# Optimization experiments

Hardware: AMD Instinct MI355X
Metric: run time of the kernel (lower is better)

Reference implementation:

```python
import jax, jax.numpy as jnp
import numpy as np

# Problem sizes
N, D, B = 4096, 2048, 64  # nodes, feature dim, sequential samples
# LARFDSSOM hyperparameters (from __init__ defaults)
A_T = 0.3          # activation threshold
DSBETA = 1e-4      # moving-average rate
E_B = 0.5          # winner learning rate
E_N = 0.01 * E_B   # neighbor learning rate (e_n is multiplied by e_b in __init__)
EPS_DS = 0.01      # relevance smoothing


def setup_inputs() -> dict:
    key = jax.random.key(0)
    k0, k1, k2, k3, k4 = jax.random.split(key, 5)
    return {
        "x": jax.random.uniform(k0, (B, D), jnp.float32),
        "weights": jax.random.uniform(k1, (N, D), jnp.float32),
        "moving_avg": jax.random.uniform(k2, (N, D), jnp.float32),
        "relevances": jax.random.uniform(k3, (N, D), jnp.float32),
        "wins": jnp.zeros((N,), jnp.float32),
        "neighbors": jax.random.randint(k4, (N, N), 0, 2) > 0,
    }


def _som_steps(x, weights, moving_avg, relevances, wins, neighbors):
    """Sequential LARFDSSOM update_map over B samples (codebook at max size,
    so the add_node branch is structurally impossible and the per-sample step
    is either 'update winner + neighbors' or a no-op)."""
    node_ids = jnp.arange(weights.shape[0])

    def step(state, w):
        W, M, R, wn = state
        diff = w[None, :] - W                          # [N, D]
        # weighted_distance + activation
        dists = jnp.sum(R * diff * diff, axis=1)       # [N]
        rel_sum = jnp.sum(R, axis=1)                   # [N]
        act = rel_sum / (rel_sum + dists + 1e-7)
        winner = jnp.argmax(act)
        do_upd = act[winner] >= A_T                    # else no-op (codebook full)
        is_winner = node_ids == winner
        is_nb = neighbors[winner] & (~is_winner)
        # per-node learning rate: e_b for winner, e_n for neighbors, 0 otherwise
        lr = jnp.where(is_winner, E_B, jnp.where(is_nb, E_N, 0.0))[:, None]  # [N, 1]
        # update_node (vectorized over all nodes, masked below)
        dist_abs = jnp.abs(diff)
        M_new = lr * DSBETA * dist_abs + (1.0 - lr * DSBETA) * M
        mx = jnp.max(M_new, axis=1, keepdims=True)
        mn = jnp.min(M_new, axis=1, keepdims=True)
        av = jnp.mean(M_new, axis=1, keepdims=True)
        denom = EPS_DS * (mx - mn)
        # denom == 0 -> original produces NaN then sets relevance to 1.0
        arg = jnp.clip((M_new - av) / jnp.where(denom == 0.0, 1.0, denom), -80.0, 80.0)
        R_new = jnp.where(denom == 0.0, 1.0, 1.0 / (1.0 + jnp.exp(arg)))
        W_new = W + lr * diff
        m = (do_upd & (lr[:, 0] > 0.0))[:, None]       # rows actually touched
        W = jnp.where(m, W_new, W)
        M = jnp.where(m, M_new, M)
        R = jnp.where(m, R_new, R)
        wn = wn + jnp.where(is_winner & do_upd, 1.0, 0.0)
        return (W, M, R, wn), None

    (W, M, R, wn), _ = jax.lax.scan(step, (weights, moving_avg, relevances, wins), x)
    return W


def reference(x, weights, moving_avg, relevances, wins, neighbors):
    return _som_steps(x, weights, moving_avg, relevances, wins, neighbors)
```

## Files before the change

### kernel.cpp

```cpp
#include <hip/hip_runtime.h>
#include <cstddef>

#define NN 4096
#define DD 2048
#define BB 64
#define RPB 8
#define NBLK (NN / RPB)

constexpr float kAT     = 0.3f;
constexpr float kDSBETA = 1e-4f;
constexpr float kEB     = 0.5f;
constexpr float kEN     = 0.005f;
constexpr float kEPS    = 0.01f;

__device__ __forceinline__ float wave_sum_f(float v) {
#pragma unroll
    for (int o = 32; o; o >>= 1) v += __shfl_xor(v, o, 64);
    return v;
}
__device__ __forceinline__ double wave_sum_d(double v) {
#pragma unroll
    for (int o = 32; o; o >>= 1) v += __shfl_xor(v, o, 64);
    return v;
}
__device__ __forceinline__ float wave_max_f(float v) {
#pragma unroll
    for (int o = 32; o; o >>= 1) v = fmaxf(v, __shfl_xor(v, o, 64));
    return v;
}
__device__ __forceinline__ float wave_min_f(float v) {
#pragma unroll
    for (int o = 32; o; o >>= 1) v = fminf(v, __shfl_xor(v, o, 64));
    return v;
}
__device__ __forceinline__ unsigned long long wave_max_u64(unsigned long long v) {
#pragma unroll
    for (int o = 32; o; o >>= 1) {
        const unsigned long long u = __shfl_xor(v, o, 64);
        v = (u > v) ? u : v;
    }
    return v;
}

__global__ void detect_nb(const unsigned char* __restrict__ nb, unsigned* __restrict__ flag) {
    unsigned v = 0;
    const int i0 = threadIdx.x * 256;
    for (int i = 0; i < 256; i++) {
        const int idx = i0 + i;
        if ((idx & 3) != 0) v |= nb[idx];
    }
    if (v != 0) atomicOr(flag, 1u);
}

__global__ __launch_bounds__(256, 2) void som_persist(
    const float* __restrict__ x,
    const float* __restrict__ W0,
    const float* __restrict__ M0,
    const float* __restrict__ R0,
    const unsigned char* __restrict__ nbb,
    const unsigned* __restrict__ flag,
    float* __restrict__ Wout,
    unsigned long long* __restrict__ part,
    unsigned* __restrict__ cnt)
{
    const int tid  = threadIdx.x;
    const int wid  = tid >> 6;
    const int lane = tid & 63;
    const int n0   = (int)blockIdx.x * RPB;
    const int col  = tid * 8;

    __shared__ double sdd[2][RPB][4];
    __shared__ float  sf[3][4];
    __shared__ unsigned long long skk[RPB];
    __shared__ unsigned long long sKey;

    const bool nb_byte = (*flag != 0);
    const int* nbi = (const int*)nbb;

    float w[RPB][8], r[RPB][8], m[RPB][8], xcur[8];

#pragma unroll
    for (int row = 0; row < RPB; ++row) {
        const size_t base = (size_t)(n0 + row) * DD + col;
        *(float4*)(&w[row][0]) = *(const float4*)(W0 + base);
        *(float4*)(&w[row][4]) = *(const float4*)(W0 + base + 4);
        *(float4*)(&r[row][0]) = *(const float4*)(R0 + base);
        *(float4*)(&r[row][4]) = *(const float4*)(R0 + base + 4);
        *(float4*)(&m[row][0]) = *(const float4*)(M0 + base);
        *(float4*)(&m[row][4]) = *(const float4*)(M0 + base + 4);
    }
    *(float4*)(xcur)     = *(const float4*)(x + col);
    *(float4*)(xcur + 4) = *(const float4*)(x + col + 4);

    auto act_phase = [&](int slot) {
#pragma unroll
        for (int row = 0; row < RPB; ++row) {
            double pd = 0.0, ps = 0.0;
#pragma unroll
            for (int j = 0; j < 8; ++j) {
                const double d  = (double)xcur[j] - (double)w[row][j];
                const double rj = (double)r[row][j];
                pd += rj * d * d;
                ps += rj;
            }
            pd = wave_sum_d(pd); ps = wave_sum_d(ps);
            if (lane == 0) { sdd[0][row][wid] = pd; sdd[1][row][wid] = ps; }
        }
        __syncthreads();
        if (tid < RPB) {
            const int row = tid;
            const double td = sdd[0][row][0] + sdd[0][row][1] + sdd[0][row][2] + sdd[0][row][3];
            const double tr = sdd[1][row][0] + sdd[1][row][1] + sdd[1][row][2] + sdd[1][row][3];
            const double act = tr / (tr + td + 1e-7);
            const unsigned long long ab = (unsigned long long)__double_as_longlong(act);
            skk[row] = (ab & ~0xFFFULL) | (unsigned long long)(4095 - (n0 + row));
        }
        __syncthreads();
        if (tid == 0) {
            unsigned long long k = skk[0];
#pragma unroll
            for (int i = 1; i < RPB; ++i) k = (skk[i] > k) ? skk[i] : k;
            atomicMax(&part[((size_t)slot * 64 + (blockIdx.x & 63)) * 8], k);
            __hip_atomic_fetch_add(&cnt[((size_t)slot * 8 + (blockIdx.x & 7)) * 16], 1u,
                                   __ATOMIC_RELEASE, __HIP_MEMORY_SCOPE_AGENT);
        }
        __syncthreads();
    };

    act_phase(0);

    for (int t = 0; t < BB; ++t) {
        if (wid == 0) {
            int it = 0;
            while (true) {
                unsigned c = 0;
                if (lane < 8)
                    c = __hip_atomic_load(&cnt[((size_t)t * 8 + lane) * 16],
                                          __ATOMIC_ACQUIRE, __HIP_MEMORY_SCOPE_AGENT);
                c += __shfl_xor(c, 1, 64);
                c += __shfl_xor(c, 2, 64);
                c += __shfl_xor(c, 4, 64);
                c = __shfl(c, 0, 64);
                if (c >= (unsigned)NBLK) break;
                if (++it > 2000000) break;
                __builtin_amdgcn_s_sleep(2);
            }
            unsigned long long k = __hip_atomic_load(
                &part[((size_t)t * 64 + lane) * 8],
                __ATOMIC_RELAXED, __HIP_MEMORY_SCOPE_AGENT);
            k = wave_max_u64(k);
            if (lane == 0) sKey = k;
        }
        __syncthreads();
        const unsigned long long k = sKey;
        __syncthreads();
        const double act_w = __longlong_as_double((long long)(k & ~0xFFFULL));
        const int winner   = 4095 - (int)(k & 0xFFFULL);

        if (act_w >= (double)kAT) {
#pragma unroll
            for (int row = 0; row < RPB; ++row) {
                const int n = n0 + row;
                float lr = 0.0f;
                if (n == winner) {
                    lr = kEB;
                } else {
                    const size_t off = (size_t)winner * NN + n;
                    const bool isnb = nb_byte ? (nbb[off] != 0) : (nbi[off] != 0);
                    if (isnb) lr = kEN;
                }
                if (lr != 0.0f) {
                    const float c1 = lr * kDSBETA;
                    const float c2 = 1.0f - c1;
                    float psum = 0.0f, pmx = -INFINITY, pmn = INFINITY;
#pragma unroll
                    for (int j = 0; j < 8; ++j) {
                        const float d  = xcur[j] - w[row][j];
                        const float mv = c1 * fabsf(d) + c2 * m[row][j];
                        w[row][j] += lr * d;
                        m[row][j] = mv;
                        psum += mv;
                        pmx = fmaxf(pmx, mv);
                        pmn = fminf(pmn, mv);
                    }
                    psum = wave_sum_f(psum); pmx = wave_max_f(pmx); pmn = wave_min_f(pmn);
                    if (lane == 0) { sf[0][wid] = psum; sf[1][wid] = pmx; sf[2][wid] = pmn; }
                    __syncthreads();
                    const float ts  = sf[0][0] + sf[0][1] + sf[0][2] + sf[0][3];
                    const float tmx = fmaxf(fmaxf(sf[1][0], sf[1][1]), fmaxf(sf[1][2], sf[1][3]));
                    const float tmn = fminf(fminf(sf[2][0], sf[2][1]), fminf(sf[2][2], sf[2][3]));
                    __syncthreads();
                    const float av    = ts * (1.0f / (float)DD);
                    const float denom = kEPS * (tmx - tmn);
                    if (denom == 0.0f) {
#pragma unroll
                        for (int j = 0; j < 8; ++j) r[row][j] = 1.0f;
                    } else {
#pragma unroll
                        for (int j = 0; j < 8; ++j) {
                            float a = (m[row][j] - av) / denom;
                            a = fminf(fmaxf(a, -80.0f), 80.0f);
                            r[row][j] = 1.0f / (1.0f + expf(a));
                        }
                    }
                }
            }
        }

        if (t < BB - 1) {
            const size_t xb = (size_t)(t + 1) * DD + col;
            *(float4*)(xcur)     = *(const float4*)(x + xb);
            *(float4*)(xcur + 4) = *(const float4*)(x + xb + 4);
            act_phase(t + 1);
        }
    }

#pragma unroll
    for (int row = 0; row < RPB; ++row) {
        const size_t base = (size_t)(n0 + row) * DD + col;
        *(float4*)(Wout + base)     = *(float4*)(&w[row][0]);
        *(float4*)(Wout + base + 4) = *(float4*)(&w[row][4]);
    }
}

__global__ __launch_bounds__(256) void som_step(
    const float* __restrict__ x_upd, const float* __restrict__ x_act,
    float* __restrict__ W, float* __restrict__ M, float* __restrict__ R,
    const void* __restrict__ nb, const unsigned* __restrict__ flag,
    const unsigned long long* __restrict__ part_upd,
    unsigned long long* __restrict__ part_act)
{
    const int n   = blockIdx.x;
    const int tid = threadIdx.x;
    __shared__ float  sred[3][4];
    __shared__ double sredd[2][4];

    float lr = 0.0f;
    if (part_upd != nullptr) {
        unsigned long long k = part_upd[(size_t)(tid & 63) * 8];
        k = wave_max_u64(k);
        const double act_w = __longlong_as_double((long long)(k & ~0xFFFULL));
        const int winner   = 4095 - (int)(k & 0xFFFULL);
        if (act_w >= (double)kAT) {
            if (n == winner) lr = kEB;
            else {
                const size_t off = (size_t)winner * NN + n;
                const bool isnb = (*flag != 0)
                    ? (((const unsigned char*)nb)[off] != 0)
                    : (((const int*)nb)[off] != 0);
                if (isnb) lr = kEN;
            }
        }
    }
    const bool next = (x_act != nullptr);
    if (lr == 0.0f && !next) return;

    const size_t rowoff = (size_t)n * DD + (size_t)tid * 8;
    const size_t xoff   = (size_t)tid * 8;
    float w[8], r[8];
    *(float4*)(w)     = *(const float4*)(W + rowoff);
    *(float4*)(w + 4) = *(const float4*)(W + rowoff + 4);

    if (lr != 0.0f) {
        float m[8], xu[8], mnew[8];
        *(float4*)(m)      = *(const float4*)(M + rowoff);
        *(float4*)(m + 4)  = *(const float4*)(M + rowoff + 4);
        *(float4*)(xu)     = *(const float4*)(x_upd + xoff);
        *(float4*)(xu + 4) = *(const float4*)(x_upd + xoff + 4);
        const float c1 = lr * kDSBETA, c2 = 1.0f - c1;
        float psum = 0.0f, pmx = -INFINITY, pmn = INFINITY;
#pragma unroll
        for (int j = 0; j < 8; j++) {
            const float d = xu[j] - w[j];
            w[j] += lr * d;
            const float mv = c1 * fabsf(d) + c2 * m[j];
            mnew[j] = mv; psum += mv;
            pmx = fmaxf(pmx, mv); pmn = fminf(pmn, mv);
        }
        psum = wave_sum_f(psum); pmx = wave_max_f(pmx); pmn = wave_min_f(pmn);
        const int wid = tid >> 6, lane = tid & 63;
        if (lane == 0) { sred[0][wid] = psum; sred[1][wid] = pmx; sred[2][wid] = pmn; }
        __syncthreads();
        const float ts  = sred[0][0] + sred[0][1] + sred[0][2] + sred[0][3];
        const float tmx = fmaxf(fmaxf(sred[1][0], sred[1][1]), fmaxf(sred[1][2], sred[1][3]));
        const float tmn = fminf(fminf(sred[2][0], sred[2][1]), fminf(sred[2][2], sred[2][3]));
        __syncthreads();
        const float av = ts * (1.0f / (float)DD);
        const float denom = kEPS * (tmx - tmn);
        if (denom == 0.0f) {
#pragma unroll
            for (int j = 0; j < 8; j++) r[j] = 1.0f;
        } else {
#pragma unroll
            for (int j = 0; j < 8; j++) {
                float a = (mnew[j] - av) / denom;
                a = fminf(fmaxf(a, -80.0f), 80.0f);
                r[j] = 1.0f / (1.0f + expf(a));
            }
        }
        *(float4*)(W + rowoff)     = *(float4*)(w);
        *(float4*)(W + rowoff + 4) = *(float4*)(w + 4);
        *(float4*)(M + rowoff)     = *(float4*)(mnew);
        *(float4*)(M + rowoff + 4) = *(float4*)(mnew + 4);
        *(float4*)(R + rowoff)     = *(float4*)(r);
        *(float4*)(R + rowoff + 4) = *(float4*)(r + 4);
    } else {
        *(float4*)(r)     = *(const float4*)(R + rowoff);
        *(float4*)(r + 4) = *(const float4*)(R + rowoff + 4);
    }

    if (next) {
        float xn[8];
        *(float4*)(xn)     = *(const float4*)(x_act + xoff);
        *(float4*)(xn + 4) = *(const float4*)(x_act + xoff + 4);
        double pd = 0.0, ps = 0.0;
#pragma unroll
        for (int j = 0; j < 8; j++) {
            const double d  = (double)xn[j] - (double)w[j];
            const double rj = (double)r[j];
            pd += rj * d * d; ps += rj;
        }
        pd = wave_sum_d(pd); ps = wave_sum_d(ps);
        const int wid = tid >> 6, lane = tid & 63;
        if (lane == 0) { sredd[0][wid] = pd; sredd[1][wid] = ps; }
        __syncthreads();
        if (tid == 0) {
            const double td = sredd[0][0] + sredd[0][1] + sredd[0][2] + sredd[0][3];
            const double tr = sredd[1][0] + sredd[1][1] + sredd[1][2] + sredd[1][3];
            const double act = tr / (tr + td + 1e-7);
            const unsigned long long ab = (unsigned long long)__double_as_longlong(act);
            const unsigned long long kk = (ab & ~0xFFFULL) | (unsigned long long)(4095 - n);
            atomicMax(&part_act[(size_t)(n & 63) * 8], kk);
        }
    }
}

extern "C" void kernel_launch(void* const* d_in, const int* in_sizes, int n_in,
                              void* d_out, int out_size, void* d_ws, size_t ws_size,
                              hipStream_t stream) {
    const float*         x   = (const float*)d_in[0];
    const float*         W0  = (const float*)d_in[1];
    float*               M   = (float*)d_in[2];
    float*               R   = (float*)d_in[3];
    const unsigned char* nbb = (const unsigned char*)d_in[5];
    float*               W   = (float*)d_out;

    unsigned long long* part = (unsigned long long*)d_ws;
    const size_t part_bytes  = (size_t)66 * 64 * 8 * sizeof(unsigned long long);
    unsigned* cnt   = (unsigned*)((char*)d_ws + part_bytes);
    const size_t cnt_bytes = (size_t)BB * 8 * 16 * sizeof(unsigned);
    unsigned* flagp = (unsigned*)((char*)d_ws + part_bytes + cnt_bytes);

    hipMemsetAsync(d_ws, 0, part_bytes + cnt_bytes + 64, stream);
    detect_nb<<<1, 256, 0, stream>>>(nbb, flagp);

    int occ = 0;
    hipError_t qerr = hipOccupancyMaxActiveBlocksPerMultiprocessor(
        &occ, (const void*)som_persist, 256, 0);
    if (qerr == hipSuccess && occ >= 2) {
        som_persist<<<NBLK, 256, 0, stream>>>(x, W0, M, R, nbb, flagp, W, part, cnt);
        return;
    }

    hipMemcpyAsync(W, W0, sizeof(float) * (size_t)NN * DD, hipMemcpyDeviceToDevice, stream);
    som_step<<<NN, 256, 0, stream>>>(nullptr, x, W, M, R, nbb, flagp, nullptr, part);
    for (int t = 0; t < BB; t++) {
        const float* xu = x + (size_t)t * DD;
        const float* xa = (t < BB - 1) ? (x + (size_t)(t + 1) * DD) : nullptr;
        const unsigned long long* pu = part + (size_t)t * 64 * 8;
        unsigned long long*       pa = (t < BB - 1) ? (part + (size_t)(t + 1) * 64 * 8) : nullptr;
        som_step<<<NN, 256, 0, stream>>>(xu, xa, W, M, R, nbb, flagp, pu, pa);
    }
}
```

Baseline: 1.681 ms.

## Replace atomic counter barrier with per-block key slots and block-0 broadcast

The grid-wide winner reduction no longer has every block atomicMax into shared partials, bump a counter, and then spin on it. Each block now stores its max key into its own slot. Block 0 polls all 512 slots until none is zero, reduces them, and publishes the winner to 8 replicated broadcast words that the other blocks spin on. This is meant to cut atomic contention and the latency of the per-step global barrier, at the cost of a two-hop handoff through block 0 and relaxed-ordering loads that treat a zero key as not yet written.

Measured after the change: 1.686 ms. About the same (+0.3%).

```diff
diff --git a/kernel.cpp b/kernel.cpp
--- a/kernel.cpp
+++ b/kernel.cpp
@@ -60,13 +60,14 @@
     const unsigned char* __restrict__ nbb,
     const unsigned* __restrict__ flag,
     float* __restrict__ Wout,
-    unsigned long long* __restrict__ part,
-    unsigned* __restrict__ cnt)
+    unsigned long long* __restrict__ pkey,
+    unsigned long long* __restrict__ bcast)
 {
     const int tid  = threadIdx.x;
     const int wid  = tid >> 6;
     const int lane = tid & 63;
-    const int n0   = (int)blockIdx.x * RPB;
+    const int bid  = (int)blockIdx.x;
+    const int n0   = bid * RPB;
     const int col  = tid * 8;
 
     __shared__ double sdd[2][RPB][4];
@@ -120,9 +121,8 @@
             unsigned long long k = skk[0];
 #pragma unroll
             for (int i = 1; i < RPB; ++i) k = (skk[i] > k) ? skk[i] : k;
-            atomicMax(&part[((size_t)slot * 64 + (blockIdx.x & 63)) * 8], k);
-            __hip_atomic_fetch_add(&cnt[((size_t)slot * 8 + (blockIdx.x & 7)) * 16], 1u,
-                                   __ATOMIC_RELEASE, __HIP_MEMORY_SCOPE_AGENT);
+            __hip_atomic_store(&pkey[(size_t)slot * NBLK + bid], k,
+                               __ATOMIC_RELAXED, __HIP_MEMORY_SCOPE_AGENT);
         }
         __syncthreads();
     };
@@ -131,25 +131,40 @@
 
     for (int t = 0; t < BB; ++t) {
         if (wid == 0) {
-            int it = 0;
-            while (true) {
-                unsigned c = 0;
+            unsigned long long kmax = 0;
+            if (bid == 0) {
+                unsigned long long* pk = pkey + (size_t)t * NBLK;
+                unsigned long long kk[8];
+                int it = 0;
+                while (true) {
+                    bool miss = false;
+#pragma unroll
+                    for (int i = 0; i < 8; ++i) {
+                        kk[i] = __hip_atomic_load(&pk[lane + 64 * i],
+                                                  __ATOMIC_RELAXED, __HIP_MEMORY_SCOPE_AGENT);
+                        miss |= (kk[i] == 0ull);
+                    }
+                    if (!__any(miss)) break;
+                    if (++it > 2000000) break;
+                    __builtin_amdgcn_s_sleep(1);
+                }
+#pragma unroll
+                for (int i = 0; i < 8; ++i) kmax = (kk[i] > kmax) ? kk[i] : kmax;
+                kmax = wave_max_u64(kmax);
                 if (lane < 8)
-                    c = __hip_atomic_load(&cnt[((size_t)t * 8 + lane) * 16],
-                                          __ATOMIC_ACQUIRE, __HIP_MEMORY_SCOPE_AGENT);
-                c += __shfl_xor(c, 1, 64);
-                c += __shfl_xor(c, 2, 64);
-                c += __shfl_xor(c, 4, 64);
-                c = __shfl(c, 0, 64);
-                if (c >= (unsigned)NBLK) break;
-                if (++it > 2000000) break;
-                __builtin_amdgcn_s_sleep(2);
-            }
-            unsigned long long k = __hip_atomic_load(
-                &part[((size_t)t * 64 + lane) * 8],
-                __ATOMIC_RELAXED, __HIP_MEMORY_SCOPE_AGENT);
-            k = wave_max_u64(k);
-            if (lane == 0) sKey = k;
+                    __hip_atomic_store(&bcast[((size_t)t * 8 + lane) * 8], kmax,
+                                       __ATOMIC_RELAXED, __HIP_MEMORY_SCOPE_AGENT);
+            } else {
+                const int rep = bid & 7;
+                int it = 0;
+                while ((kmax = __hip_atomic_load(&bcast[((size_t)t * 8 + rep) * 8],
+                                                 __ATOMIC_RELAXED, __HIP_MEMORY_SCOPE_AGENT))
+                       == 0ull) {
+                    if (++it > 2000000) break;
+                    __builtin_amdgcn_s_sleep(4);
+                }
+            }
+            if (lane == 0) sKey = kmax;
         }
         __syncthreads();
         const unsigned long long k = sKey;
@@ -347,7 +362,7 @@
 
     unsigned long long* part = (unsigned long long*)d_ws;
     const size_t part_bytes  = (size_t)66 * 64 * 8 * sizeof(unsigned long long);
-    unsigned* cnt   = (unsigned*)((char*)d_ws + part_bytes);
+    unsigned long long* bcast = (unsigned long long*)((char*)d_ws + part_bytes);
     const size_t cnt_bytes = (size_t)BB * 8 * 16 * sizeof(unsigned);
     unsigned* flagp = (unsigned*)((char*)d_ws + part_bytes + cnt_bytes);
 
@@ -358,7 +373,7 @@
     hipError_t qerr = hipOccupancyMaxActiveBlocksPerMultiprocessor(
         &occ, (const void*)som_persist, 256, 0);
     if (qerr == hipSuccess && occ >= 2) {
-        som_persist<<<NBLK, 256, 0, stream>>>(x, W0, M, R, nbb, flagp, W, part, cnt);
+        som_persist<<<NBLK, 256, 0, stream>>>(x, W0, M, R, nbb, flagp, W, part, bcast);
         return;
     }
 
```
